# Performance work log

Hardware: AMD Instinct MI355X
Metric: run time of the kernel (lower is better)

## Reference

```python
import jax, jax.numpy as jnp
import numpy as np

N = 50000      # nodes
E = 400000     # directed edges (self-loops added inside reference, per PyG default)
DIN = 256
DH = 32
HEADS = 8
DOUT = 40
SLOPE = 0.2    # GATv2Conv negative_slope default


def _gatv2_layer(x, src, dst, Wl, bl, Wr, br, att, bias, heads, out_ch):
    """One GATv2Conv (concat=True). x:[n,din], src/dst:[e], att:[heads,out_ch]."""
    n = x.shape[0]
    xl = (x @ Wl + bl).reshape(n, heads, out_ch)   # source transform
    xr = (x @ Wr + br).reshape(n, heads, out_ch)   # target transform
    e = jax.nn.leaky_relu(xl[src] + xr[dst], SLOPE)          # [e, H, C]
    s = jnp.einsum('ehc,hc->eh', e, att)                     # per-edge attention logits
    smax = jax.ops.segment_max(s, dst, num_segments=n)       # stable softmax over in-edges
    ex = jnp.exp(s - smax[dst])
    denom = jax.ops.segment_sum(ex, dst, num_segments=n)
    alpha = ex / denom[dst]                                  # [e, H]
    out = jax.ops.segment_sum(alpha[:, :, None] * xl[src], dst, num_segments=n)
    return out.reshape(n, heads * out_ch) + bias


def setup_inputs() -> dict:
    key = jax.random.key(0)
    ks = jax.random.split(key, 8)
    def gl(k, shape, fan_in):
        return jax.random.normal(k, shape, jnp.float32) * np.float32(1.0 / np.sqrt(fan_in))
    return {
        'x': jax.random.normal(ks[0], (N, DIN), jnp.float32),
        'edge_index': jax.random.randint(ks[1], (2, E), 0, N, jnp.int32),
        'W1l': gl(ks[2], (DIN, HEADS * DH), DIN),
        'b1l': jnp.zeros((HEADS * DH,), jnp.float32),
        'W1r': gl(ks[3], (DIN, HEADS * DH), DIN),
        'b1r': jnp.zeros((HEADS * DH,), jnp.float32),
        'att1': gl(ks[4], (HEADS, DH), DH),
        'bias1': jnp.zeros((HEADS * DH,), jnp.float32),
        'W2l': gl(ks[5], (HEADS * DH, DOUT), HEADS * DH),
        'b2l': jnp.zeros((DOUT,), jnp.float32),
        'W2r': gl(ks[6], (HEADS * DH, DOUT), HEADS * DH),
        'b2r': jnp.zeros((DOUT,), jnp.float32),
        'att2': gl(ks[7], (1, DOUT), DOUT),
        'bias2': jnp.zeros((DOUT,), jnp.float32),
    }


def reference(x, edge_index, W1l, b1l, W1r, b1r, att1, bias1,
              W2l, b2l, W2r, b2r, att2, bias2):
    n = x.shape[0]
    loop = jnp.arange(n, dtype=edge_index.dtype)  # add_self_loops=True (PyG default)
    src = jnp.concatenate([edge_index[0], loop])
    dst = jnp.concatenate([edge_index[1], loop])
    # eval mode: F.dropout is identity; normalization='none' -> Identity
    h = _gatv2_layer(x, src, dst, W1l, b1l, W1r, b1r, att1, bias1, HEADS, DH)
    h = jax.nn.elu(h)
    out = _gatv2_layer(h, src, dst, W2l, b2l, W2r, b2r, att2, bias2, 1, DOUT)
    return jax.nn.log_softmax(out, axis=1)
```

## Files before the change

kernel.cpp:

```cpp
#include <hip/hip_runtime.h>
#include <math.h>

#define NODES 50000
#define NEDGE 400000
#define ETOT  450000
#define DIN   256
#define C1    256
#define C2    40
#define SCAN_NB ((NODES + 255) / 256)
#define CSRCAP  600064

typedef __attribute__((ext_vector_type(8))) short bfrag;
typedef __attribute__((ext_vector_type(4))) float facc;

#define GPTR(p) (const __attribute__((address_space(1))) unsigned int*)(p)
#define LPTR(p) (__attribute__((address_space(3))) unsigned int*)(p)

static __device__ __forceinline__ float bitsf(unsigned int x) {
    float f;
    __builtin_memcpy(&f, &x, 4);
    return f;
}
static __device__ __forceinline__ unsigned short f2bf(float f) {
    unsigned int x;
    __builtin_memcpy(&x, &f, 4);
    unsigned int r = x + 0x7fffu + ((x >> 16) & 1u);
    return (unsigned short)(r >> 16);
}
static __device__ __forceinline__ float fexp2(float x) {
#if __has_builtin(__builtin_amdgcn_exp2f)
    return __builtin_amdgcn_exp2f(x);
#else
    return exp2f(x);
#endif
}

__global__ __launch_bounds__(256)
void cvt_bf16(const float* __restrict__ in, unsigned short* __restrict__ out, int n8) {
    int i = blockIdx.x * 256 + threadIdx.x;
    if (i >= n8) return;
    const float4* p = (const float4*)in + (size_t)i * 2;
    float4 u0 = p[0], u1 = p[1];
    bfrag pk;
    pk[0] = (short)f2bf(u0.x); pk[1] = (short)f2bf(u0.y);
    pk[2] = (short)f2bf(u0.z); pk[3] = (short)f2bf(u0.w);
    pk[4] = (short)f2bf(u1.x); pk[5] = (short)f2bf(u1.y);
    pk[6] = (short)f2bf(u1.z); pk[7] = (short)f2bf(u1.w);
    *(bfrag*)(out + (size_t)i * 8) = pk;
}

__global__ void count_kernel(const int* __restrict__ dstRow, int* __restrict__ cnt) {
    int e = blockIdx.x * blockDim.x + threadIdx.x;
    if (e >= ETOT) return;
    int d = (e < NEDGE) ? dstRow[e] : (e - NEDGE);
    atomicAdd(&cnt[d], 1);
}

__global__ __launch_bounds__(256)
void scan_blk(const int* __restrict__ cnt, int* __restrict__ off, int* __restrict__ blkTot) {
    __shared__ int buf[256];
    const int t = threadIdx.x;
    const int i = blockIdx.x * 256 + t;
    int v = (i < NODES) ? ((cnt[i] + 3) & ~3) : 0;
    buf[t] = v;
    __syncthreads();
    #pragma unroll
    for (int d = 1; d < 256; d <<= 1) {
        int add = (t >= d) ? buf[t - d] : 0;
        __syncthreads();
        buf[t] += add;
        __syncthreads();
    }
    if (i < NODES) off[i] = buf[t] - v;
    if (t == 255) blkTot[blockIdx.x] = buf[255];
}

__global__ __launch_bounds__(256)
void scan_top(const int* __restrict__ blkTot, int* __restrict__ blkOff, int* __restrict__ offEnd) {
    __shared__ int buf[256];
    const int t = threadIdx.x;
    int v = (t < SCAN_NB) ? blkTot[t] : 0;
    buf[t] = v;
    __syncthreads();
    #pragma unroll
    for (int d = 1; d < 256; d <<= 1) {
        int add = (t >= d) ? buf[t - d] : 0;
        __syncthreads();
        buf[t] += add;
        __syncthreads();
    }
    if (t < SCAN_NB) blkOff[t] = buf[t] - v;
    if (t == 255) *offEnd = buf[255];
}

__global__ __launch_bounds__(256)
void scan_fix(int* __restrict__ off, int* __restrict__ wrk, const int* __restrict__ blkOff) {
    const int i = blockIdx.x * 256 + threadIdx.x;
    if (i < NODES) {
        int v = off[i] + blkOff[blockIdx.x];
        off[i] = v;
        wrk[i] = v;
    }
}

__global__ void place_kernel(const int* __restrict__ srcRow, const int* __restrict__ dstRow,
                             int* __restrict__ wrk, int* __restrict__ csr) {
    int e = blockIdx.x * blockDim.x + threadIdx.x;
    if (e >= ETOT) return;
    int d, s;
    if (e < NEDGE) { d = dstRow[e]; s = srcRow[e]; }
    else           { d = e - NEDGE; s = d; }
    int slot = atomicAdd(&wrk[d], 1);
    csr[slot] = s;
}

__global__ void prep_w(const float* __restrict__ Wl, const float* __restrict__ Wr,
                       unsigned short* __restrict__ Wt, int K, int Nhalf) {
    int idx = blockIdx.x * 256 + threadIdx.x;
    int n = idx / K;
    int k = idx - n * K;
    if (n >= 2 * Nhalf) return;
    float v = (n < Nhalf) ? Wl[(size_t)k * Nhalf + n] : Wr[(size_t)k * Nhalf + (n - Nhalf)];
    Wt[idx] = f2bf(v);
}

#define GBM 128
#define GBN 128
#define GBK 32

template<typename OUTT, bool SWZ>
__global__ __launch_bounds__(256)
void mfma_gemm(const unsigned short* __restrict__ Ab, const unsigned short* __restrict__ Bt,
               const float* __restrict__ bl, const float* __restrict__ br,
               OUTT* __restrict__ Cl, OUTT* __restrict__ Cr,
               int M, int Nrows, int Nhalf, int nbnShift)
{
    __shared__ __align__(16) unsigned short As[3][GBM * GBK];
    __shared__ __align__(16) unsigned short Bs[3][GBN * GBK];

    const int tid  = threadIdx.x;
    const int lane = tid & 63;
    const int w    = tid >> 6;
    const int wr   = w >> 1;
    const int wc   = w & 1;

    int tile;
    if constexpr (SWZ) {
        const int nwg = gridDim.x;
        const int q = nwg >> 3, r = nwg & 7;
        const int xcd = blockIdx.x & 7;
        const int idx = blockIdx.x >> 3;
        tile = (xcd < r ? xcd * (q + 1) : r * (q + 1) + (xcd - r) * q) + idx;
    } else {
        tile = blockIdx.x;
    }
    const int bx   = tile >> nbnShift;
    const int by   = tile & ((1 << nbnShift) - 1);
    const int row0 = bx * GBM;
    const int col0 = by * GBN;

    facc acc[4][4];
    #pragma unroll
    for (int i = 0; i < 4; ++i)
        #pragma unroll
        for (int j = 0; j < 4; ++j) {
            facc z = {0.f, 0.f, 0.f, 0.f};
            acc[i][j] = z;
        }

    const int rA  = lane >> 2;
    const int kgA = (lane & 3) ^ ((rA >> 1) & 3);
    const int fr    = lane & 15;
    const int sRead = (lane >> 4) ^ ((fr >> 1) & 3);

    #define STAGE(bufi, k0)                                                     \
    {                                                                           \
        _Pragma("unroll")                                                       \
        for (int p = 0; p < 2; ++p) {                                           \
            const int chunk = p * 4 + w;                                        \
            const int r_loc = chunk * 16 + rA;                                  \
            const int ga = min(row0 + r_loc, M - 1);                            \
            __builtin_amdgcn_global_load_lds(                                   \
                GPTR(Ab + (size_t)ga * 256 + (k0) + kgA * 8),                   \
                LPTR(&As[bufi][chunk * 512]), 16, 0, 0);                        \
            const int gb = min(col0 + r_loc, Nrows - 1);                        \
            __builtin_amdgcn_global_load_lds(                                   \
                GPTR(Bt + (size_t)gb * 256 + (k0) + kgA * 8),                   \
                LPTR(&Bs[bufi][chunk * 512]), 16, 0, 0);                        \
        }                                                                       \
    }

    #define KSTEP(T, WSTR)                                                      \
    {                                                                           \
        asm volatile("s_waitcnt vmcnt(" WSTR ")" ::: "memory");                 \
        __builtin_amdgcn_s_barrier();                                           \
        __builtin_amdgcn_sched_barrier(0);                                      \
        constexpr int cur = (T) % 3;                                            \
        bfrag af[4], bfv[4];                                                    \
        _Pragma("unroll")                                                       \
        for (int mi = 0; mi < 4; ++mi)                                          \
            af[mi] = *(const bfrag*)(&As[cur][(wr * 64 + mi * 16 + fr) * 32 + sRead * 8]); \
        _Pragma("unroll")                                                       \
        for (int ni = 0; ni < 4; ++ni)                                          \
            bfv[ni] = *(const bfrag*)(&Bs[cur][(wc * 64 + ni * 16 + fr) * 32 + sRead * 8]); \
        if constexpr ((T) + 2 < 8) STAGE(((T) + 2) % 3, ((T) + 2) * GBK);       \
        _Pragma("unroll")                                                       \
        for (int mi = 0; mi < 4; ++mi)                                          \
            _Pragma("unroll")                                                   \
            for (int ni = 0; ni < 4; ++ni)                                      \
                acc[mi][ni] = __builtin_amdgcn_mfma_f32_16x16x32_bf16(          \
                    af[mi], bfv[ni], acc[mi][ni], 0, 0, 0);                     \
    }

    STAGE(0, 0 * GBK);
    STAGE(1, 1 * GBK);
    KSTEP(0, "4"); KSTEP(1, "4"); KSTEP(2, "4"); KSTEP(3, "4");
    KSTEP(4, "4"); KSTEP(5, "4"); KSTEP(6, "4"); KSTEP(7, "0");
    #undef KSTEP
    #undef STAGE

    #pragma unroll
    for (int mi = 0; mi < 4; ++mi) {
        const int rbase = row0 + wr * 64 + mi * 16 + ((lane >> 4) << 2);
        #pragma unroll
        for (int ni = 0; ni < 4; ++ni) {
            const int col = col0 + wc * 64 + ni * 16 + (lane & 15);
            #pragma unroll
            for (int rg = 0; rg < 4; ++rg) {
                int r = rbase + rg;
                if (r >= M) continue;
                float v = acc[mi][ni][rg];
                if (col < Nhalf) {
                    v += bl[col];
                    if constexpr (sizeof(OUTT) == 2)
                        Cl[(size_t)r * Nhalf + col] = (OUTT)f2bf(v);
                    else
                        Cl[(size_t)r * Nhalf + col] = (OUTT)v;
                } else if (col < 2 * Nhalf) {
                    int c2 = col - Nhalf;
                    v += br[c2];
                    if constexpr (sizeof(OUTT) == 2)
                        Cr[(size_t)r * Nhalf + c2] = (OUTT)f2bf(v);
                    else
                        Cr[(size_t)r * Nhalf + c2] = (OUTT)v;
                }
            }
        }
    }
}

__global__ __launch_bounds__(256)
void fused_l1(const int* __restrict__ off, const int* __restrict__ deg,
              const int* __restrict__ csr, const unsigned short* __restrict__ xl,
              const unsigned short* __restrict__ xr, const float* __restrict__ att,
              const float* __restrict__ bias, unsigned short* __restrict__ hout)
{
    const int lane = threadIdx.x & 63;
    const int n    = blockIdx.x * 4 + (threadIdx.x >> 6);
    if (n >= NODES) return;

    const int a  = __builtin_amdgcn_readfirstlane(off[n]);
    const int dn = __builtin_amdgcn_readfirstlane(deg[n]);
    const int np = (dn + 3) & ~3;

    const uint2 xrn = *(const uint2*)(xr + (size_t)n * C1 + lane * 4);
    const float xr0 = bitsf(xrn.x << 16), xr1 = bitsf(xrn.x & 0xffff0000u);
    const float xr2 = bitsf(xrn.y << 16), xr3 = bitsf(xrn.y & 0xffff0000u);
    const float4 wv = *(const float4*)(att + lane * 4);
    const float L2E = 1.4426950408889634f;
    const float w6_0 = wv.x * (0.6f * L2E), w4_0 = wv.x * (0.4f * L2E);
    const float w6_1 = wv.y * (0.6f * L2E), w4_1 = wv.y * (0.4f * L2E);
    const float w6_2 = wv.z * (0.6f * L2E), w4_2 = wv.z * (0.4f * L2E);
    const float w6_3 = wv.w * (0.6f * L2E), w4_3 = wv.w * (0.4f * L2E);

    float m = -INFINITY, d = 0.f;
    float a0 = 0.f, a1 = 0.f, a2 = 0.f, a3 = 0.f;

    uint2 R[4];
    {
        const int4 s4 = *(const int4*)(csr + a);
        R[0] = *(const uint2*)(xl + (size_t)s4.x * C1 + lane * 4);
        R[1] = *(const uint2*)(xl + (size_t)s4.y * C1 + lane * 4);
        R[2] = *(const uint2*)(xl + (size_t)s4.z * C1 + lane * 4);
        R[3] = *(const uint2*)(xl + (size_t)s4.w * C1 + lane * 4);
    }

    for (int i = 0; i < np; i += 4) {
        uint2 Rn[4];
        const int nx = (i + 4 < np) ? (i + 4) : i;
        {
            const int4 s4 = *(const int4*)(csr + a + nx);
            Rn[0] = *(const uint2*)(xl + (size_t)s4.x * C1 + lane * 4);
            Rn[1] = *(const uint2*)(xl + (size_t)s4.y * C1 + lane * 4);
            Rn[2] = *(const uint2*)(xl + (size_t)s4.z * C1 + lane * 4);
            Rn[3] = *(const uint2*)(xl + (size_t)s4.w * C1 + lane * 4);
        }

        float x0[4], x1[4], x2[4], x3[4], p[4];
        #pragma unroll
        for (int k = 0; k < 4; ++k) {
            x0[k] = bitsf(R[k].x << 16);
            x1[k] = bitsf(R[k].x & 0xffff0000u);
            x2[k] = bitsf(R[k].y << 16);
            x3[k] = bitsf(R[k].y & 0xffff0000u);
            const float v0 = x0[k] + xr0, v1 = x1[k] + xr1;
            const float v2 = x2[k] + xr2, v3 = x3[k] + xr3;
            float pp;
            pp = w6_0 * v0;
            pp = fmaf(w4_0, fabsf(v0), pp);
            pp = fmaf(w6_1, v1, pp);
            pp = fmaf(w4_1, fabsf(v1), pp);
            pp = fmaf(w6_2, v2, pp);
            pp = fmaf(w4_2, fabsf(v2), pp);
            pp = fmaf(w6_3, v3, pp);
            pp = fmaf(w4_3, fabsf(v3), pp);
            pp += __shfl_xor(pp, 1);
            pp += __shfl_xor(pp, 2);
            pp += __shfl_xor(pp, 4);
            p[k] = (i + k < dn) ? pp : -INFINITY;
        }

        const float pm = fmaxf(fmaxf(p[0], p[1]), fmaxf(p[2], p[3]));
        if (__any(pm > m + 8.f)) {
            #pragma unroll
            for (int k = 0; k < 4; ++k) {
                const float mN = fmaxf(m, p[k]);
                const float sc = fexp2(m - mN);
                const float wg = fexp2(p[k] - mN);
                m = mN;
                d = fmaf(d, sc, wg);
                a0 = fmaf(wg, x0[k], a0 * sc);
                a1 = fmaf(wg, x1[k], a1 * sc);
                a2 = fmaf(wg, x2[k], a2 * sc);
                a3 = fmaf(wg, x3[k], a3 * sc);
            }
        } else {
            #pragma unroll
            for (int k = 0; k < 4; ++k) {
                const float wg = fexp2(p[k] - m);
                d += wg;
                a0 = fmaf(wg, x0[k], a0);
                a1 = fmaf(wg, x1[k], a1);
                a2 = fmaf(wg, x2[k], a2);
                a3 = fmaf(wg, x3[k], a3);
            }
        }

        #pragma unroll
        for (int k = 0; k < 4; ++k) R[k] = Rn[k];
    }

    const float inv = 1.f / d;
    const float4 bv = *(const float4*)(bias + lane * 4);
    float v0 = fmaf(a0, inv, bv.x), v1 = fmaf(a1, inv, bv.y);
    float v2 = fmaf(a2, inv, bv.z), v3 = fmaf(a3, inv, bv.w);
    v0 = v0 > 0.f ? v0 : (fexp2(v0 * L2E) - 1.f);
    v1 = v1 > 0.f ? v1 : (fexp2(v1 * L2E) - 1.f);
    v2 = v2 > 0.f ? v2 : (fexp2(v2 * L2E) - 1.f);
    v3 = v3 > 0.f ? v3 : (fexp2(v3 * L2E) - 1.f);
    uint2 o;
    o.x = (unsigned int)f2bf(v0) | ((unsigned int)f2bf(v1) << 16);
    o.y = (unsigned int)f2bf(v2) | ((unsigned int)f2bf(v3) << 16);
    *(uint2*)(hout + (size_t)n * C1 + lane * 4) = o;
}

__global__ __launch_bounds__(256)
void fused_l2(const int* __restrict__ off, const int* __restrict__ deg,
              const int* __restrict__ csr, const float* __restrict__ h2l,
              const float* __restrict__ h2r, const float* __restrict__ att,
              const float* __restrict__ bias, float* __restrict__ out)
{
    const int lane = threadIdx.x & 63;
    const int n    = blockIdx.x * 4 + (threadIdx.x >> 6);
    if (n >= NODES) return;
    const int l8 = lane & 7;
    const int g  = lane >> 3;

    const int a  = __builtin_amdgcn_readfirstlane(off[n]);
    const int dn = __builtin_amdgcn_readfirstlane(deg[n]);
    const float L2E = 1.4426950408889634f;

    float w6[5], w4[5], xr[5];
    #pragma unroll
    for (int j = 0; j < 5; ++j) {
        const int c = l8 + 8 * j;
        const float w = att[c];
        w6[j] = w * (0.6f * L2E);
        w4[j] = w * (0.4f * L2E);
        xr[j] = h2r[(size_t)n * C2 + c];
    }

    float m = -INFINITY, dl = 0.f;
    float acc[5] = {0.f, 0.f, 0.f, 0.f, 0.f};

    float R[5];
    {
        const int src = csr[a + g];
        const float* row = h2l + (size_t)src * C2 + l8;
        #pragma unroll
        for (int j = 0; j < 5; ++j) R[j] = row[8 * j];
    }

    for (int c0 = 0; c0 < dn; c0 += 8) {
        float Rn[5];
        {
            const int nx = (c0 + 8 < dn) ? (c0 + 8) : c0;
            const int src = csr[a + nx + g];
            const float* row = h2l + (size_t)src * C2 + l8;
            #pragma unroll
            for (int j = 0; j < 5; ++j) Rn[j] = row[8 * j];
        }

        const int idx = c0 + g;
        float p = 0.f;
        #pragma unroll
        for (int j = 0; j < 5; ++j) {
            const float v = R[j] + xr[j];
            p = fmaf(w6[j], v, p);
            p = fmaf(w4[j], fabsf(v), p);
        }
        p += __shfl_xor(p, 1);
        p += __shfl_xor(p, 2);
        p += __shfl_xor(p, 4);
        if (idx >= dn) p = -INFINITY;

        if (__any(p > m + 8.f)) {
            float pm = p;
            pm = fmaxf(pm, __shfl_xor(pm, 8));
            pm = fmaxf(pm, __shfl_xor(pm, 16));
            pm = fmaxf(pm, __shfl_xor(pm, 32));
            const float mN = fmaxf(m, pm);
            const float sc = fexp2(m - mN);
            const float wg = fexp2(p - mN);
            m = mN;
            dl = fmaf(dl, sc, wg);
            #pragma unroll
            for (int j = 0; j < 5; ++j) acc[j] = fmaf(wg, R[j], acc[j] * sc);
        } else {
            const float wg = fexp2(p - m);
            dl += wg;
            #pragma unroll
            for (int j = 0; j < 5; ++j) acc[j] = fmaf(wg, R[j], acc[j]);
        }

        #pragma unroll
        for (int j = 0; j < 5; ++j) R[j] = Rn[j];
    }

    #pragma unroll
    for (int o = 8; o < 64; o <<= 1) {
        dl += __shfl_xor(dl, o);
        #pragma unroll
        for (int j = 0; j < 5; ++j) acc[j] += __shfl_xor(acc[j], o);
    }

    const float inv = 1.f / dl;
    float v[5];
    float mx = -INFINITY;
    #pragma unroll
    for (int j = 0; j < 5; ++j) {
        v[j] = fmaf(acc[j], inv, bias[l8 + 8 * j]);
        mx = fmaxf(mx, v[j]);
    }
    mx = fmaxf(mx, __shfl_xor(mx, 1));
    mx = fmaxf(mx, __shfl_xor(mx, 2));
    mx = fmaxf(mx, __shfl_xor(mx, 4));
    float s = 0.f;
    #pragma unroll
    for (int j = 0; j < 5; ++j) s += fexp2((v[j] - mx) * L2E);
    s += __shfl_xor(s, 1);
    s += __shfl_xor(s, 2);
    s += __shfl_xor(s, 4);
    const float lg = logf(s);
    if (g == 0) {
        #pragma unroll
        for (int j = 0; j < 5; ++j)
            out[(size_t)n * C2 + l8 + 8 * j] = v[j] - mx - lg;
    }
}

extern "C" void kernel_launch(void* const* d_in, const int* in_sizes, int n_in,
                              void* d_out, int out_size, void* d_ws, size_t ws_size,
                              hipStream_t stream)
{
    const float* x     = (const float*)d_in[0];
    const int*   ei    = (const int*)  d_in[1];
    const float* W1l   = (const float*)d_in[2];
    const float* b1l   = (const float*)d_in[3];
    const float* W1r   = (const float*)d_in[4];
    const float* b1r   = (const float*)d_in[5];
    const float* att1  = (const float*)d_in[6];
    const float* bias1 = (const float*)d_in[7];
    const float* W2l   = (const float*)d_in[8];
    const float* b2l   = (const float*)d_in[9];
    const float* W2r   = (const float*)d_in[10];
    const float* b2r   = (const float*)d_in[11];
    const float* att2  = (const float*)d_in[12];
    const float* bias2 = (const float*)d_in[13];
    float* out = (float*)d_out;

    float* ws = (float*)d_ws;
    unsigned short* xl1 = (unsigned short*)ws;
    unsigned short* xr1 = (unsigned short*)(ws + 6400000);
    unsigned short* xb  = (unsigned short*)(ws + 12800000);
    int*   csr    = (int*)(ws + 19200000);
    int*   off    = csr + CSRCAP;
    int*   cnt    = off + (NODES + 1);
    int*   wrk    = cnt + NODES;
    int*   blkTot = wrk + NODES;
    int*   blkOff = blkTot + SCAN_NB;
    unsigned short* Wt1 = (unsigned short*)(ws + 19960000);
    unsigned short* Wt2 = (unsigned short*)(ws + 20030000);
    unsigned short* h = xr1;
    float* h2l = ws;
    float* h2r = ws + 2000000;

    const int* srcRow = ei;
    const int* dstRow = ei + NEDGE;

    hipMemsetAsync(cnt, 0, NODES * sizeof(int), stream);
    hipMemsetAsync(csr, 0, CSRCAP * sizeof(int), stream);
    count_kernel<<<(ETOT + 255) / 256, 256, 0, stream>>>(dstRow, cnt);
    scan_blk<<<SCAN_NB, 256, 0, stream>>>(cnt, off, blkTot);
    scan_top<<<1, 256, 0, stream>>>(blkTot, blkOff, off + NODES);
    scan_fix<<<SCAN_NB, 256, 0, stream>>>(off, wrk, blkOff);
    place_kernel<<<(ETOT + 255) / 256, 256, 0, stream>>>(srcRow, dstRow, wrk, csr);

    cvt_bf16<<<(NODES * DIN / 8 + 255) / 256, 256, 0, stream>>>(x, xb, NODES * DIN / 8);
    prep_w<<<(512 * 256 + 255) / 256, 256, 0, stream>>>(W1l, W1r, Wt1, DIN, C1);
    prep_w<<<(80 * 256 + 255) / 256, 256, 0, stream>>>(W2l, W2r, Wt2, C1, C2);

    mfma_gemm<unsigned short, true><<<((NODES + GBM - 1) / GBM) * 4, 256, 0, stream>>>(
        xb, Wt1, b1l, b1r, xl1, xr1, NODES, 2 * C1, C1, 2);
    fused_l1<<<(NODES + 3) / 4, 256, 0, stream>>>(off, cnt, csr, xl1, xr1, att1, bias1, h);

    mfma_gemm<float, false><<<(NODES + GBM - 1) / GBM, 256, 0, stream>>>(
        h, Wt2, b2l, b2r, h2l, h2r, NODES, 2 * C2, C2, 0);
    fused_l2<<<(NODES + 3) / 4, 256, 0, stream>>>(off, cnt, csr, h2l, h2r, att2, bias2, out);
}
```

Before: 209.6 us.

## Replace layer-1 GEMM with weight-stationary register-resident B kernel

New measurement: 221.0 us. 1.05x slower.

```diff
diff --git a/kernel.cpp b/kernel.cpp
--- a/kernel.cpp
+++ b/kernel.cpp
@@ -122,6 +122,118 @@
     if (n >= 2 * Nhalf) return;
     float v = (n < Nhalf) ? Wl[(size_t)k * Nhalf + n] : Wr[(size_t)k * Nhalf + (n - Nhalf)];
     Wt[idx] = f2bf(v);
+}
+
+#define PAN 64
+#define PPB 2
+
+__global__ __launch_bounds__(256, 2)
+void gemm1_ws(const unsigned short* __restrict__ Ab, const unsigned short* __restrict__ Bt,
+              const float* __restrict__ bl, const float* __restrict__ br,
+              unsigned short* __restrict__ Cl, unsigned short* __restrict__ Cr,
+              int M, int Nhalf)
+{
+    __shared__ __align__(16) unsigned short As[2][PAN * 256];
+
+    const int lane = threadIdx.x & 63;
+    const int w    = threadIdx.x >> 6;
+    const int fr   = lane & 15;
+    const int hi   = lane >> 4;
+
+    const int nwg = gridDim.x;
+    const int q = nwg >> 3, r = nwg & 7;
+    const int bid = ((blockIdx.x & 7) < r
+                         ? (blockIdx.x & 7) * (q + 1)
+                         : r * (q + 1) + ((blockIdx.x & 7) - r) * q) + (blockIdx.x >> 3);
+    const int cb    = bid & 1;
+    const int mc    = bid >> 1;
+    const int col0  = cb * 256 + w * 64;
+    const int prow0 = mc * (PAN * PPB);
+
+    bfrag bf[4][8];
+    #pragma unroll
+    for (int ni = 0; ni < 4; ++ni) {
+        const unsigned short* bp = Bt + (size_t)(col0 + ni * 16 + fr) * 256 + hi * 8;
+        #pragma unroll
+        for (int kk = 0; kk < 8; ++kk)
+            bf[ni][kk] = *(const bfrag*)(bp + kk * 32);
+    }
+
+    #define STAGE1(bufi, prow)                                                  \
+    {                                                                           \
+        _Pragma("unroll")                                                       \
+        for (int j = 0; j < 8; ++j) {                                           \
+            const int c  = w * 8 + j;                                           \
+            const int rl = c * 2 + (lane >> 5);                                 \
+            const int kg = (lane & 31) ^ (rl & 7);                              \
+            const int grow = min((prow) + rl, M - 1);                           \
+            __builtin_amdgcn_global_load_lds(                                   \
+                GPTR(Ab + (size_t)grow * 256 + kg * 8),                         \
+                LPTR(&As[bufi][c * 512]), 16, 0, 0);                            \
+        }                                                                       \
+    }
+
+    STAGE1(0, prow0);
+
+    #pragma unroll
+    for (int p = 0; p < PPB; ++p) {
+        asm volatile("s_waitcnt vmcnt(0)" ::: "memory");
+        __builtin_amdgcn_s_barrier();
+        __builtin_amdgcn_sched_barrier(0);
+        if (p + 1 < PPB) STAGE1((p + 1) & 1, prow0 + (p + 1) * PAN);
+
+        facc acc[4][4];
+        #pragma unroll
+        for (int i = 0; i < 4; ++i)
+            #pragma unroll
+            for (int j = 0; j < 4; ++j) {
+                facc z = {0.f, 0.f, 0.f, 0.f};
+                acc[i][j] = z;
+            }
+
+        const unsigned short* asb = &As[p & 1][0];
+        #pragma unroll
+        for (int kk = 0; kk < 8; ++kk) {
+            bfrag af[4];
+            #pragma unroll
+            for (int mi = 0; mi < 4; ++mi) {
+                const int rr = mi * 16 + fr;
+                const int kg = (kk * 4 + hi) ^ (rr & 7);
+                af[mi] = *(const bfrag*)(asb + rr * 256 + kg * 8);
+            }
+            #pragma unroll
+            for (int mi = 0; mi < 4; ++mi)
+                #pragma unroll
+                for (int ni = 0; ni < 4; ++ni)
+                    acc[mi][ni] = __builtin_amdgcn_mfma_f32_16x16x32_bf16(
+                        af[mi], bf[ni][kk], acc[mi][ni], 0, 0, 0);
+        }
+
+        const int prow = prow0 + p * PAN;
+        #pragma unroll
+        for (int mi = 0; mi < 4; ++mi) {
+            const int rbase = prow + mi * 16 + (hi << 2);
+            #pragma unroll
+            for (int ni = 0; ni < 4; ++ni) {
+                const int col = col0 + ni * 16 + fr;
+                #pragma unroll
+                for (int rg = 0; rg < 4; ++rg) {
+                    const int rr = rbase + rg;
+                    if (rr >= M) continue;
+                    float v = acc[mi][ni][rg];
+                    if (col < Nhalf) {
+                        v += bl[col];
+                        Cl[(size_t)rr * Nhalf + col] = f2bf(v);
+                    } else {
+                        const int c2 = col - Nhalf;
+                        v += br[c2];
+                        Cr[(size_t)rr * Nhalf + c2] = f2bf(v);
+                    }
+                }
+            }
+        }
+    }
+    #undef STAGE1
 }
 
 #define GBM 128
@@ -530,8 +642,8 @@
     prep_w<<<(512 * 256 + 255) / 256, 256, 0, stream>>>(W1l, W1r, Wt1, DIN, C1);
     prep_w<<<(80 * 256 + 255) / 256, 256, 0, stream>>>(W2l, W2r, Wt2, C1, C2);
 
-    mfma_gemm<unsigned short, true><<<((NODES + GBM - 1) / GBM) * 4, 256, 0, stream>>>(
-        xb, Wt1, b1l, b1r, xl1, xr1, NODES, 2 * C1, C1, 2);
+    gemm1_ws<<<((NODES + PAN * PPB - 1) / (PAN * PPB)) * 2, 256, 0, stream>>>(
+        xb, Wt1, b1l, b1r, xl1, xr1, NODES, C1);
     fused_l1<<<(NODES + 3) / 4, 256, 0, stream>>>(off, cnt, csr, xl1, xr1, att1, bias1, h);
 
     mfma_gemm<float, false><<<(NODES + GBM - 1) / GBM, 256, 0, stream>>>(
```
